# Performance work log

Measured on AMD Instinct MI355X. Metric: run time of the kernel, lower is better.

The kernel has to match this reference:

```python
import jax, jax.numpy as jnp
import numpy as np

N, E, C, H, G = 100000, 1600000, 128, 64, 512
TOL = 1e-7          # PyG topk tolerance
MIN_SCORE = 0.05
EPS_KL = 1e-14


def setup_inputs() -> dict:
    key = jax.random.key(0)
    ks = jax.random.split(key, 12)
    d = {}
    d["x"] = jax.random.normal(ks[0], (N, C), jnp.float32)
    d["edge_index"] = jax.random.randint(ks[1], (2, E), 0, N)
    d["batch"] = jnp.sort(jax.random.randint(ks[2], (N,), 0, G))
    d["attn"] = jax.random.uniform(ks[3], (N,), jnp.float32, minval=1e-3, maxval=1.0)
    def lin(k, i, o):
        return (jax.random.normal(k, (i, o), jnp.float32) / np.sqrt(i)).astype(jnp.float32)
    d["W1"] = lin(ks[4], C, H); d["b1"] = jnp.zeros((H,), jnp.float32)
    d["W2"] = lin(ks[5], H, H); d["b2"] = jnp.zeros((H,), jnp.float32)
    d["pool_w"] = (jax.random.normal(ks[6], (C,), jnp.float32) / np.sqrt(C)).astype(jnp.float32)
    d["W3"] = lin(ks[7], H, H); d["b3"] = jnp.zeros((H,), jnp.float32)
    d["W4"] = lin(ks[8], H, H); d["b4"] = jnp.zeros((H,), jnp.float32)
    d["Wl"] = lin(ks[9], H, 1); d["bl"] = jnp.zeros((1,), jnp.float32)
    return d


def _gin(x, src, dst, Wa, ba, Wb, bb, edge_w=None):
    # GINConv with eps=0: nn((1+0)*x + sum_{j in N(i)} x_j), nn = Lin-ReLU-Lin
    msg = x[src]                                   # [E, F] gather
    if edge_w is not None:
        msg = msg * edge_w[:, None]                # drop pruned edges
    agg = jax.ops.segment_sum(msg, dst, num_segments=x.shape[0])
    h = x + agg
    return jax.nn.relu(h @ Wa + ba) @ Wb + bb


def reference(x, edge_index, batch, attn, W1, b1, W2, b2, pool_w, W3, b3, W4, b4, Wl, bl):
    src, dst = edge_index[0], edge_index[1]
    out = jax.nn.relu(_gin(x, src, dst, W1, b1, W2, b2))

    # --- TopKPooling(min_score=0.05), attn=x ---
    raw = x @ pool_w                               # [N] attention logits
    m = jax.ops.segment_max(raw, batch, num_segments=G)
    e = jnp.exp(raw - m[batch])
    z = jax.ops.segment_sum(e, batch, num_segments=G)
    score = e / z[batch]                           # per-graph softmax
    smax = jax.ops.segment_max(score, batch, num_segments=G)
    thresh = jnp.minimum(smax[batch] - TOL, MIN_SCORE)
    mask = score > thresh                          # kept nodes (>=1 per graph)
    maskf = mask.astype(x.dtype)
    out = out * (score * maskf)[:, None]           # x[perm] * score[perm]
    edge_keep = maskf[src] * maskf[dst]            # filter_adj: both endpoints kept

    out = jax.nn.relu(_gin(out, src, dst, W3, b3, W4, b4, edge_w=edge_keep)) * maskf[:, None]
    graph_out = jax.ops.segment_sum(out, batch, num_segments=G)  # global_add_pool
    pred = (graph_out @ Wl + bl).reshape(-1)       # [G]

    # attn_loss = scatter_mean(kl_div(log(score+eps), attn[perm]), batch)
    kl = attn * (jnp.log(attn) - jnp.log(score + EPS_KL))
    cnt = jax.ops.segment_sum(maskf, batch, num_segments=G)
    attn_loss = jax.ops.segment_sum(kl * maskf, batch, num_segments=G) / jnp.maximum(cnt, 1.0)

    ratio = maskf.sum() / x.shape[0]
    return pred, attn_loss, ratio
```

## Files before the change

kernel.cpp:

```cpp
#include <hip/hip_runtime.h>
#include <math.h>

#define N_NODES 100000
#define N_EDGES 1600000
#define C_IN    128
#define H_DIM   64
#define G_GRAPHS 512
#define MAXG    4096
#define ELCAP   65536
#define KPG     32
#define NBITS   3136

__device__ __forceinline__ int lbound(const int* __restrict__ b, int val) {
    int lo = 0, hi = N_NODES;
    while (lo < hi) {
        int mid = (lo + hi) >> 1;
        if (b[mid] < val) lo = mid + 1; else hi = mid;
    }
    return lo;
}

__global__ void kpre(const float* __restrict__ x, const float* __restrict__ pool_w,
                     float* __restrict__ sc, unsigned int* __restrict__ zero_region) {
    int gid = blockIdx.x * blockDim.x + threadIdx.x;
    if (gid < NBITS + 1) zero_region[gid] = 0u;
    const int lane = threadIdx.x & 63;
    const int l32  = lane & 31;
    const int half = lane >> 5;
    const float4 pwv = ((const float4*)pool_w)[l32];
    const int wid = blockIdx.x * (blockDim.x >> 6) + (threadIdx.x >> 6);
    const int nw  = gridDim.x * (blockDim.x >> 6);
    for (int r0 = wid * 4; r0 < N_NODES; r0 += nw * 4) {
        int rowA = r0 + half;
        int rowB = r0 + 2 + half;
        float4 xa = ((const float4*)(x + (size_t)rowA * C_IN))[l32];
        float4 xb = ((const float4*)(x + (size_t)rowB * C_IN))[l32];
        float pa = xa.x * pwv.x + xa.y * pwv.y + xa.z * pwv.z + xa.w * pwv.w;
        float pb = xb.x * pwv.x + xb.y * pwv.y + xb.z * pwv.z + xb.w * pwv.w;
        #pragma unroll
        for (int m = 16; m > 0; m >>= 1) {
            pa += __shfl_xor(pa, m, 64);
            pb += __shfl_xor(pb, m, 64);
        }
        if (l32 == 0) { sc[rowA] = pa; sc[rowB] = pb; }
    }
}

__device__ __forceinline__ float blk_max(float v, float* red, int lane, int w) {
    #pragma unroll
    for (int m = 32; m > 0; m >>= 1) v = fmaxf(v, __shfl_xor(v, m, 64));
    if (lane == 0) red[w] = v;
    __syncthreads();
    float r = fmaxf(fmaxf(red[0], red[1]), fmaxf(red[2], red[3]));
    __syncthreads();
    return r;
}
__device__ __forceinline__ float blk_sum(float v, float* red, int lane, int w) {
    #pragma unroll
    for (int m = 32; m > 0; m >>= 1) v += __shfl_xor(v, m, 64);
    if (lane == 0) red[w] = v;
    __syncthreads();
    float r = (red[0] + red[1]) + (red[2] + red[3]);
    __syncthreads();
    return r;
}

__global__ void kA4(const int* __restrict__ batch, const float* __restrict__ attn,
                    float* __restrict__ sc, unsigned int* __restrict__ kept_bits,
                    int* __restrict__ klist, int* __restrict__ kcnt,
                    float* __restrict__ B, float* __restrict__ out) {
    __shared__ float buf[MAXG];
    __shared__ float red[4];
    __shared__ int   lst[KPG];
    __shared__ int   cntk;
    const int g = blockIdx.x;
    const int t = threadIdx.x;
    const int lane = t & 63;
    const int w = t >> 6;
    const int ns = lbound(batch, g);
    const int ne = lbound(batch, g + 1);
    const int cn = ne - ns;
    if (cn <= 0) {
        if (t == 0) { out[G_GRAPHS + g] = 0.f; kcnt[g] = 0; }
        return;
    }
    if (t == 0) cntk = 0;
    float lmax = -3.4e38f;
    for (int i = t; i < cn; i += 256) { float r = sc[ns + i]; buf[i] = r; lmax = fmaxf(lmax, r); }
    float m = blk_max(lmax, red, lane, w);
    float lsum = 0.f;
    for (int i = t; i < cn; i += 256) { float e = expf(buf[i] - m); buf[i] = e; lsum += e; }
    float z = blk_sum(lsum, red, lane, w);
    float thresh = fminf(1.f / z - 1e-7f, 0.05f);
    float klacc = 0.f;
    for (int i = t; i < cn; i += 256) {
        float s = buf[i] / z;
        if (s > thresh) {
            int n = ns + i;
            int p = atomicAdd(&cntk, 1);
            if (p < KPG) lst[p] = i;
            sc[n] = s;
            float a = attn[n];
            klacc += a * (logf(a) - logf(s + 1e-14f));
        }
    }
    float klsum = blk_sum(klacc, red, lane, w);
    int kct = cntk;
    int kc = kct < KPG ? kct : KPG;
    if (t == 0) {
        out[G_GRAPHS + g] = (kct > 0) ? klsum / (float)kct : 0.f;
        kcnt[g] = kc;
    }
    for (int i = t; i < kc; i += 256) {
        int n = ns + lst[i];
        klist[g * KPG + i] = n;
        atomicOr(&kept_bits[n >> 5], 1u << (n & 31));
    }
    for (int j = t; j < kc * H_DIM; j += 256)
        B[(size_t)(ns + lst[j >> 6]) * H_DIM + (j & 63)] = 0.f;
}

__device__ __forceinline__ void emit(bool hit, int s, int d, int* __restrict__ list,
                                     int cap, int* __restrict__ count, int lane) {
    unsigned long long bal = __ballot(hit);
    if (bal == 0ull) return;
    int leader = __ffsll((long long)bal) - 1;
    int cnt = __popcll(bal);
    int base = 0;
    if (lane == leader) base = atomicAdd(count, cnt);
    base = __shfl(base, leader, 64);
    if (hit) {
        int p = base + __popcll(bal & ((1ull << lane) - 1ull));
        if (p < cap) { list[p] = s; list[cap + p] = d; }
    }
}

__global__ void k5f2(const int* __restrict__ ei, const unsigned int* __restrict__ bits,
                     const float* __restrict__ x, const float* __restrict__ W1,
                     float* __restrict__ B, int* __restrict__ elsd,
                     int* __restrict__ elcount) {
    __shared__ float W1s[C_IN * H_DIM];
    __shared__ int ls[1024], ld[1024];
    __shared__ int c1;
    const int t = threadIdx.x;
    const int lane = t & 63;
    if (t == 0) c1 = 0;
    int t4 = blockIdx.x * 256 + t;
    bool valid = t4 < (N_EDGES / 4);
    int4 s4 = make_int4(0, 0, 0, 0), d4 = make_int4(0, 0, 0, 0);
    if (valid) {
        s4 = ((const int4*)ei)[t4];
        d4 = ((const int4*)(ei + N_EDGES))[t4];
    }
    __syncthreads();
    int sv[4] = {s4.x, s4.y, s4.z, s4.w};
    int dv[4] = {d4.x, d4.y, d4.z, d4.w};
    bool bk[4];
    #pragma unroll
    for (int q = 0; q < 4; ++q) {
        int ss = sv[q], dd = dv[q];
        bool kd = valid && (((bits[dd >> 5] >> (dd & 31)) & 1u) != 0u);
        bk[q] = kd && (((bits[ss >> 5] >> (ss & 31)) & 1u) != 0u);
        if (kd) { int p = atomicAdd(&c1, 1); ls[p] = ss; ld[p] = dd; }
    }
    #pragma unroll
    for (int q = 0; q < 4; ++q) emit(bk[q], sv[q], dv[q], elsd, ELCAP, elcount, lane);
    __syncthreads();
    const int nloc = c1;
    if (nloc == 0) return;
    for (int i = t; i < C_IN * H_DIM; i += 256) W1s[i] = W1[i];
    __syncthreads();
    const int w = t >> 6;
    for (int idx = w; idx < nloc; idx += 4) {
        int s = ls[idx];
        int d = ld[idx];
        const float4* xr = (const float4*)(x + (size_t)s * C_IN);
        float acc = 0.f;
        #pragma unroll 8
        for (int k4 = 0; k4 < C_IN / 4; ++k4) {
            float4 xv = xr[k4];
            acc = fmaf(xv.x, W1s[(4 * k4 + 0) * H_DIM + lane], acc);
            acc = fmaf(xv.y, W1s[(4 * k4 + 1) * H_DIM + lane], acc);
            acc = fmaf(xv.z, W1s[(4 * k4 + 2) * H_DIM + lane], acc);
            acc = fmaf(xv.w, W1s[(4 * k4 + 3) * H_DIM + lane], acc);
        }
        atomicAdd(&B[(size_t)d * H_DIM + lane], acc);
    }
}

__device__ __forceinline__ float computeA(int n, int lane,
                                          const float* __restrict__ x,
                                          const float* __restrict__ B,
                                          const float* __restrict__ sc,
                                          const float* __restrict__ W1, float b1l,
                                          const float* __restrict__ W2, float b2l,
                                          const float* __restrict__ W3) {
    const float4* xr = (const float4*)(x + (size_t)n * C_IN);
    float u = 0.f;
    #pragma unroll 8
    for (int k4 = 0; k4 < C_IN / 4; ++k4) {
        float4 xv = xr[k4];
        u = fmaf(xv.x, W1[(4 * k4 + 0) * H_DIM + lane], u);
        u = fmaf(xv.y, W1[(4 * k4 + 1) * H_DIM + lane], u);
        u = fmaf(xv.z, W1[(4 * k4 + 2) * H_DIM + lane], u);
        u = fmaf(xv.w, W1[(4 * k4 + 3) * H_DIM + lane], u);
    }
    float t1 = fmaxf(u + B[(size_t)n * H_DIM + lane] + b1l, 0.f);
    float o1 = b2l;
    #pragma unroll 8
    for (int k = 0; k < H_DIM; ++k) o1 = fmaf(__shfl(t1, k, 64), W2[k * H_DIM + lane], o1);
    o1 = fmaxf(o1, 0.f);
    float v = 0.f;
    #pragma unroll 8
    for (int k = 0; k < H_DIM; ++k) v = fmaf(__shfl(o1, k, 64), W3[k * H_DIM + lane], v);
    return v * sc[n];
}

__global__ void k8c(const int* __restrict__ klist, const int* __restrict__ kcnt,
                    const float* __restrict__ sc, const float* __restrict__ x,
                    const float* __restrict__ W1, const float* __restrict__ b1,
                    const float* __restrict__ W2, const float* __restrict__ b2,
                    const float* __restrict__ W3, const float* __restrict__ b3,
                    const float* __restrict__ W4, const float* __restrict__ b4,
                    const float* __restrict__ Wl, const float* __restrict__ bl,
                    const float* __restrict__ B, const int* __restrict__ elsd,
                    const int* __restrict__ elcount, float* __restrict__ out) {
    const int g = blockIdx.x;
    const int lane = threadIdx.x;
    const float b1l = b1[lane], b2l = b2[lane], b3l = b3[lane], b4l = b4[lane];
    const int kc = kcnt[g];
    int ec = *elcount; if (ec > ELCAP) ec = ELCAP;
    float gsum = 0.f;
    for (int i = 0; i < kc; ++i) {
        int n = __builtin_amdgcn_readfirstlane(klist[g * KPG + i]);
        float agg = 0.f;
        for (int base = 0; base < ec; base += 64) {
            int idx = base + lane;
            int dd = (idx < ec) ? elsd[ELCAP + idx] : -1;
            bool mtc = (dd == n);
            int ssl = mtc ? elsd[idx] : 0;
            unsigned long long bal = __ballot(mtc);
            while (bal) {
                int j = __ffsll((long long)bal) - 1;
                bal &= bal - 1;
                int s = __builtin_amdgcn_readfirstlane(__shfl(ssl, j, 64));
                agg += computeA(s, lane, x, B, sc, W1, b1l, W2, b2l, W3);
            }
        }
        float vA = computeA(n, lane, x, B, sc, W1, b1l, W2, b2l, W3);
        float t = fmaxf(vA + agg + b3l, 0.f);
        float o2 = b4l;
        #pragma unroll 8
        for (int k = 0; k < H_DIM; ++k) o2 = fmaf(__shfl(t, k, 64), W4[k * H_DIM + lane], o2);
        gsum += fmaxf(o2, 0.f);
    }
    float p = gsum * Wl[lane];
    #pragma unroll
    for (int m = 32; m > 0; m >>= 1) p += __shfl_xor(p, m, 64);
    if (lane == 0) out[g] = p + bl[0];
    if (g == 0) {
        int tot = 0;
        for (int i = lane; i < G_GRAPHS; i += 64) tot += kcnt[i];
        #pragma unroll
        for (int m = 32; m > 0; m >>= 1) tot += __shfl_xor(tot, m, 64);
        if (lane == 0) out[2 * G_GRAPHS] = (float)tot * (1.f / (float)N_NODES);
    }
}

extern "C" void kernel_launch(void* const* d_in, const int* in_sizes, int n_in,
                              void* d_out, int out_size, void* d_ws, size_t ws_size,
                              hipStream_t stream) {
    const float* x      = (const float*)d_in[0];
    const int*   ei     = (const int*)d_in[1];
    const int*   batch  = (const int*)d_in[2];
    const float* attn   = (const float*)d_in[3];
    const float* W1     = (const float*)d_in[4];
    const float* b1     = (const float*)d_in[5];
    const float* W2     = (const float*)d_in[6];
    const float* b2     = (const float*)d_in[7];
    const float* pool_w = (const float*)d_in[8];
    const float* W3     = (const float*)d_in[9];
    const float* b3     = (const float*)d_in[10];
    const float* W4     = (const float*)d_in[11];
    const float* b4     = (const float*)d_in[12];
    const float* Wl     = (const float*)d_in[13];
    const float* bl     = (const float*)d_in[14];
    float* out = (float*)d_out;

    float* B      = (float*)d_ws;
    float* sc     = B + (size_t)N_NODES * H_DIM;
    int*   klist  = (int*)(sc + N_NODES);
    int*   kcnt   = klist + G_GRAPHS * KPG;
    int*   elsd   = kcnt + G_GRAPHS;
    unsigned int* kept_bits = (unsigned int*)(elsd + 2 * ELCAP);
    int*          elcount   = (int*)(kept_bits + NBITS);

    kpre <<<2048, 256, 0, stream>>>(x, pool_w, sc, kept_bits);
    kA4  <<<G_GRAPHS, 256, 0, stream>>>(batch, attn, sc, kept_bits, klist, kcnt, B, out);
    k5f2 <<<(N_EDGES / 4 + 255) / 256, 256, 0, stream>>>(ei, kept_bits, x, W1, B,
                                                         elsd, elcount);
    k8c  <<<G_GRAPHS, 64, 0, stream>>>(klist, kcnt, sc, x, W1, b1, W2, b2, W3, b3,
                                       W4, b4, Wl, bl, B, elsd, elcount, out);
}
```

Baseline: 174.9 us.

## Fuse pooling, edge filtering and second GIN into one cooperative kernel

```diff
diff --git a/kernel.cpp b/kernel.cpp
--- a/kernel.cpp
+++ b/kernel.cpp
@@ -1,5 +1,8 @@
 #include <hip/hip_runtime.h>
+#include <hip/hip_cooperative_groups.h>
 #include <math.h>
+
+namespace cg = cooperative_groups;
 
 #define N_NODES 100000
 #define N_EDGES 1600000
@@ -9,21 +12,25 @@
 #define MAXG    4096
 #define ELCAP   65536
 #define KPG     32
-#define NBITS   3136
-
-__device__ __forceinline__ int lbound(const int* __restrict__ b, int val) {
-    int lo = 0, hi = N_NODES;
-    while (lo < hi) {
-        int mid = (lo + hi) >> 1;
-        if (b[mid] < val) lo = mid + 1; else hi = mid;
-    }
-    return lo;
-}
+#define MAGIC   0x5A17C0DE
 
 __global__ void kpre(const float* __restrict__ x, const float* __restrict__ pool_w,
-                     float* __restrict__ sc, unsigned int* __restrict__ zero_region) {
+                     const int* __restrict__ batch, float* __restrict__ sc,
+                     int* __restrict__ gstart) {
     int gid = blockIdx.x * blockDim.x + threadIdx.x;
-    if (gid < NBITS + 1) zero_region[gid] = 0u;
+    int nth = gridDim.x * blockDim.x;
+    for (int i = gid; i < N_NODES; i += nth) {
+        int bc = batch[i];
+        if (i == 0) {
+            for (int g = 0; g <= bc; ++g) gstart[g] = 0;
+        } else {
+            int bp = batch[i - 1];
+            for (int g = bp + 1; g <= bc; ++g) gstart[g] = i;
+        }
+        if (i == N_NODES - 1) {
+            for (int g = bc + 1; g <= G_GRAPHS; ++g) gstart[g] = N_NODES;
+        }
+    }
     const int lane = threadIdx.x & 63;
     const int l32  = lane & 31;
     const int half = lane >> 5;
@@ -46,7 +53,7 @@
     }
 }
 
-__device__ __forceinline__ float blk_max(float v, float* red, int lane, int w) {
+__device__ __forceinline__ float blk_max(float v, volatile float* red, int lane, int w) {
     #pragma unroll
     for (int m = 32; m > 0; m >>= 1) v = fmaxf(v, __shfl_xor(v, m, 64));
     if (lane == 0) red[w] = v;
@@ -55,7 +62,7 @@
     __syncthreads();
     return r;
 }
-__device__ __forceinline__ float blk_sum(float v, float* red, int lane, int w) {
+__device__ __forceinline__ float blk_sum(float v, volatile float* red, int lane, int w) {
     #pragma unroll
     for (int m = 32; m > 0; m >>= 1) v += __shfl_xor(v, m, 64);
     if (lane == 0) red[w] = v;
@@ -63,61 +70,6 @@
     float r = (red[0] + red[1]) + (red[2] + red[3]);
     __syncthreads();
     return r;
-}
-
-__global__ void kA4(const int* __restrict__ batch, const float* __restrict__ attn,
-                    float* __restrict__ sc, unsigned int* __restrict__ kept_bits,
-                    int* __restrict__ klist, int* __restrict__ kcnt,
-                    float* __restrict__ B, float* __restrict__ out) {
-    __shared__ float buf[MAXG];
-    __shared__ float red[4];
-    __shared__ int   lst[KPG];
-    __shared__ int   cntk;
-    const int g = blockIdx.x;
-    const int t = threadIdx.x;
-    const int lane = t & 63;
-    const int w = t >> 6;
-    const int ns = lbound(batch, g);
-    const int ne = lbound(batch, g + 1);
-    const int cn = ne - ns;
-    if (cn <= 0) {
-        if (t == 0) { out[G_GRAPHS + g] = 0.f; kcnt[g] = 0; }
-        return;
-    }
-    if (t == 0) cntk = 0;
-    float lmax = -3.4e38f;
-    for (int i = t; i < cn; i += 256) { float r = sc[ns + i]; buf[i] = r; lmax = fmaxf(lmax, r); }
-    float m = blk_max(lmax, red, lane, w);
-    float lsum = 0.f;
-    for (int i = t; i < cn; i += 256) { float e = expf(buf[i] - m); buf[i] = e; lsum += e; }
-    float z = blk_sum(lsum, red, lane, w);
-    float thresh = fminf(1.f / z - 1e-7f, 0.05f);
-    float klacc = 0.f;
-    for (int i = t; i < cn; i += 256) {
-        float s = buf[i] / z;
-        if (s > thresh) {
-            int n = ns + i;
-            int p = atomicAdd(&cntk, 1);
-            if (p < KPG) lst[p] = i;
-            sc[n] = s;
-            float a = attn[n];
-            klacc += a * (logf(a) - logf(s + 1e-14f));
-        }
-    }
-    float klsum = blk_sum(klacc, red, lane, w);
-    int kct = cntk;
-    int kc = kct < KPG ? kct : KPG;
-    if (t == 0) {
-        out[G_GRAPHS + g] = (kct > 0) ? klsum / (float)kct : 0.f;
-        kcnt[g] = kc;
-    }
-    for (int i = t; i < kc; i += 256) {
-        int n = ns + lst[i];
-        klist[g * KPG + i] = n;
-        atomicOr(&kept_bits[n >> 5], 1u << (n & 31));
-    }
-    for (int j = t; j < kc * H_DIM; j += 256)
-        B[(size_t)(ns + lst[j >> 6]) * H_DIM + (j & 63)] = 0.f;
 }
 
 __device__ __forceinline__ void emit(bool hit, int s, int d, int* __restrict__ list,
@@ -132,59 +84,6 @@
     if (hit) {
         int p = base + __popcll(bal & ((1ull << lane) - 1ull));
         if (p < cap) { list[p] = s; list[cap + p] = d; }
-    }
-}
-
-__global__ void k5f2(const int* __restrict__ ei, const unsigned int* __restrict__ bits,
-                     const float* __restrict__ x, const float* __restrict__ W1,
-                     float* __restrict__ B, int* __restrict__ elsd,
-                     int* __restrict__ elcount) {
-    __shared__ float W1s[C_IN * H_DIM];
-    __shared__ int ls[1024], ld[1024];
-    __shared__ int c1;
-    const int t = threadIdx.x;
-    const int lane = t & 63;
-    if (t == 0) c1 = 0;
-    int t4 = blockIdx.x * 256 + t;
-    bool valid = t4 < (N_EDGES / 4);
-    int4 s4 = make_int4(0, 0, 0, 0), d4 = make_int4(0, 0, 0, 0);
-    if (valid) {
-        s4 = ((const int4*)ei)[t4];
-        d4 = ((const int4*)(ei + N_EDGES))[t4];
-    }
-    __syncthreads();
-    int sv[4] = {s4.x, s4.y, s4.z, s4.w};
-    int dv[4] = {d4.x, d4.y, d4.z, d4.w};
-    bool bk[4];
-    #pragma unroll
-    for (int q = 0; q < 4; ++q) {
-        int ss = sv[q], dd = dv[q];
-        bool kd = valid && (((bits[dd >> 5] >> (dd & 31)) & 1u) != 0u);
-        bk[q] = kd && (((bits[ss >> 5] >> (ss & 31)) & 1u) != 0u);
-        if (kd) { int p = atomicAdd(&c1, 1); ls[p] = ss; ld[p] = dd; }
-    }
-    #pragma unroll
-    for (int q = 0; q < 4; ++q) emit(bk[q], sv[q], dv[q], elsd, ELCAP, elcount, lane);
-    __syncthreads();
-    const int nloc = c1;
-    if (nloc == 0) return;
-    for (int i = t; i < C_IN * H_DIM; i += 256) W1s[i] = W1[i];
-    __syncthreads();
-    const int w = t >> 6;
-    for (int idx = w; idx < nloc; idx += 4) {
-        int s = ls[idx];
-        int d = ld[idx];
-        const float4* xr = (const float4*)(x + (size_t)s * C_IN);
-        float acc = 0.f;
-        #pragma unroll 8
-        for (int k4 = 0; k4 < C_IN / 4; ++k4) {
-            float4 xv = xr[k4];
-            acc = fmaf(xv.x, W1s[(4 * k4 + 0) * H_DIM + lane], acc);
-            acc = fmaf(xv.y, W1s[(4 * k4 + 1) * H_DIM + lane], acc);
-            acc = fmaf(xv.z, W1s[(4 * k4 + 2) * H_DIM + lane], acc);
-            acc = fmaf(xv.w, W1s[(4 * k4 + 3) * H_DIM + lane], acc);
-        }
-        atomicAdd(&B[(size_t)d * H_DIM + lane], acc);
     }
 }
 
@@ -216,54 +115,166 @@
     return v * sc[n];
 }
 
-__global__ void k8c(const int* __restrict__ klist, const int* __restrict__ kcnt,
-                    const float* __restrict__ sc, const float* __restrict__ x,
-                    const float* __restrict__ W1, const float* __restrict__ b1,
-                    const float* __restrict__ W2, const float* __restrict__ b2,
-                    const float* __restrict__ W3, const float* __restrict__ b3,
-                    const float* __restrict__ W4, const float* __restrict__ b4,
-                    const float* __restrict__ Wl, const float* __restrict__ bl,
-                    const float* __restrict__ B, const int* __restrict__ elsd,
-                    const int* __restrict__ elcount, float* __restrict__ out) {
+__global__ __launch_bounds__(256, 2)
+void kcoop(const int* __restrict__ batch, const float* __restrict__ attn,
+           const float* __restrict__ x, const int* __restrict__ ei,
+           const float* __restrict__ W1, const float* __restrict__ b1,
+           const float* __restrict__ W2, const float* __restrict__ b2,
+           const float* __restrict__ W3, const float* __restrict__ b3,
+           const float* __restrict__ W4, const float* __restrict__ b4,
+           const float* __restrict__ Wl, const float* __restrict__ bl,
+           const int* __restrict__ gstart, float* __restrict__ sc,
+           int* __restrict__ flags, int* __restrict__ klist, int* __restrict__ kcnt,
+           int* __restrict__ elsd, int* __restrict__ elcount,
+           float* __restrict__ B, float* __restrict__ out) {
+    __shared__ float buf[MAXG];
+    __shared__ float red[4];
+    __shared__ int   lst[KPG];
+    __shared__ int   cntk;
+    cg::grid_group grid = cg::this_grid();
     const int g = blockIdx.x;
-    const int lane = threadIdx.x;
-    const float b1l = b1[lane], b2l = b2[lane], b3l = b3[lane], b4l = b4[lane];
-    const int kc = kcnt[g];
-    int ec = *elcount; if (ec > ELCAP) ec = ELCAP;
-    float gsum = 0.f;
-    for (int i = 0; i < kc; ++i) {
-        int n = __builtin_amdgcn_readfirstlane(klist[g * KPG + i]);
-        float agg = 0.f;
-        for (int base = 0; base < ec; base += 64) {
-            int idx = base + lane;
-            int dd = (idx < ec) ? elsd[ELCAP + idx] : -1;
-            bool mtc = (dd == n);
-            int ssl = mtc ? elsd[idx] : 0;
-            unsigned long long bal = __ballot(mtc);
-            while (bal) {
-                int j = __ffsll((long long)bal) - 1;
-                bal &= bal - 1;
-                int s = __builtin_amdgcn_readfirstlane(__shfl(ssl, j, 64));
-                agg += computeA(s, lane, x, B, sc, W1, b1l, W2, b2l, W3);
-            }
-        }
-        float vA = computeA(n, lane, x, B, sc, W1, b1l, W2, b2l, W3);
-        float t = fmaxf(vA + agg + b3l, 0.f);
-        float o2 = b4l;
-        #pragma unroll 8
-        for (int k = 0; k < H_DIM; ++k) o2 = fmaf(__shfl(t, k, 64), W4[k * H_DIM + lane], o2);
-        gsum += fmaxf(o2, 0.f);
-    }
-    float p = gsum * Wl[lane];
-    #pragma unroll
-    for (int m = 32; m > 0; m >>= 1) p += __shfl_xor(p, m, 64);
-    if (lane == 0) out[g] = p + bl[0];
-    if (g == 0) {
-        int tot = 0;
-        for (int i = lane; i < G_GRAPHS; i += 64) tot += kcnt[i];
-        #pragma unroll
-        for (int m = 32; m > 0; m >>= 1) tot += __shfl_xor(tot, m, 64);
-        if (lane == 0) out[2 * G_GRAPHS] = (float)tot * (1.f / (float)N_NODES);
+    const int t = threadIdx.x;
+    const int lane = t & 63;
+    const int w = t >> 6;
+
+    if (g == 0 && t == 0) *elcount = 0;
+    const int ns = gstart[g], ne = gstart[g + 1];
+    const int cn = ne - ns;
+    if (cn > 0) {
+        if (t == 0) cntk = 0;
+        float lmax = -3.4e38f;
+        for (int i = t; i < cn; i += 256) { float r = sc[ns + i]; buf[i] = r; lmax = fmaxf(lmax, r); }
+        float m = blk_max(lmax, red, lane, w);
+        float lsum = 0.f;
+        for (int i = t; i < cn; i += 256) { float e = expf(buf[i] - m); buf[i] = e; lsum += e; }
+        float z = blk_sum(lsum, red, lane, w);
+        float thresh = fminf(1.f / z - 1e-7f, 0.05f);
+        float klacc = 0.f;
+        for (int i = t; i < cn; i += 256) {
+            float s = buf[i] / z;
+            if (s > thresh) {
+                int n = ns + i;
+                int p = atomicAdd(&cntk, 1);
+                if (p < KPG) lst[p] = i;
+                sc[n] = s;
+                float a = attn[n];
+                klacc += a * (logf(a) - logf(s + 1e-14f));
+            }
+        }
+        float klsum = blk_sum(klacc, red, lane, w);
+        int kct = cntk;
+        int kc = kct < KPG ? kct : KPG;
+        if (t == 0) {
+            out[G_GRAPHS + g] = (kct > 0) ? klsum / (float)kct : 0.f;
+            kcnt[g] = kc;
+        }
+        for (int i = t; i < kc; i += 256) {
+            int n = ns + lst[i];
+            klist[g * KPG + i] = n;
+            flags[n] = MAGIC;
+        }
+        for (int j = t; j < kc * H_DIM; j += 256)
+            B[(size_t)(ns + lst[j >> 6]) * H_DIM + (j & 63)] = 0.f;
+    } else if (t == 0) {
+        out[G_GRAPHS + g] = 0.f;
+        kcnt[g] = 0;
+    }
+    grid.sync();
+
+    {
+        __shared__ int c1;
+        int* ls = (int*)buf;
+        int* ld = ls + 1024;
+        const int niter = (N_EDGES / 4 + 255) / 256;
+        for (int it = g; it < niter; it += G_GRAPHS) {
+            if (t == 0) c1 = 0;
+            __syncthreads();
+            int t4 = it * 256 + t;
+            bool valid = t4 < (N_EDGES / 4);
+            int4 s4 = make_int4(0, 0, 0, 0), d4 = make_int4(0, 0, 0, 0);
+            if (valid) {
+                s4 = ((const int4*)ei)[t4];
+                d4 = ((const int4*)(ei + N_EDGES))[t4];
+            }
+            int sv[4] = {s4.x, s4.y, s4.z, s4.w};
+            int dv[4] = {d4.x, d4.y, d4.z, d4.w};
+            bool bk[4];
+            #pragma unroll
+            for (int q = 0; q < 4; ++q) {
+                int ss = sv[q], dd = dv[q];
+                bool kd = valid && (flags[dd] == MAGIC);
+                bk[q] = kd && (flags[ss] == MAGIC);
+                if (kd) { int p = atomicAdd(&c1, 1); ls[p] = ss; ld[p] = dd; }
+            }
+            #pragma unroll
+            for (int q = 0; q < 4; ++q) emit(bk[q], sv[q], dv[q], elsd, ELCAP, elcount, lane);
+            __syncthreads();
+            const int nloc = c1;
+            for (int idx = w; idx < nloc; idx += 4) {
+                int s = ls[idx];
+                int d = ld[idx];
+                const float4* xr = (const float4*)(x + (size_t)s * C_IN);
+                float acc = 0.f;
+                #pragma unroll 8
+                for (int k4 = 0; k4 < C_IN / 4; ++k4) {
+                    float4 xv = xr[k4];
+                    acc = fmaf(xv.x, W1[(4 * k4 + 0) * H_DIM + lane], acc);
+                    acc = fmaf(xv.y, W1[(4 * k4 + 1) * H_DIM + lane], acc);
+                    acc = fmaf(xv.z, W1[(4 * k4 + 2) * H_DIM + lane], acc);
+                    acc = fmaf(xv.w, W1[(4 * k4 + 3) * H_DIM + lane], acc);
+                }
+                atomicAdd(&B[(size_t)d * H_DIM + lane], acc);
+            }
+            __syncthreads();
+        }
+    }
+    grid.sync();
+
+    {
+        const float b1l = b1[lane], b2l = b2[lane], b3l = b3[lane], b4l = b4[lane];
+        const int kc = kcnt[g];
+        int ec = *elcount; if (ec > ELCAP) ec = ELCAP;
+        float gsum = 0.f;
+        for (int i = w; i < kc; i += 4) {
+            int n = __builtin_amdgcn_readfirstlane(klist[g * KPG + i]);
+            float agg = 0.f;
+            for (int base = 0; base < ec; base += 64) {
+                int idx = base + lane;
+                int dd = (idx < ec) ? elsd[ELCAP + idx] : -1;
+                bool mtc = (dd == n);
+                int ssl = mtc ? elsd[idx] : 0;
+                unsigned long long bal = __ballot(mtc);
+                while (bal) {
+                    int j = __ffsll((long long)bal) - 1;
+                    bal &= bal - 1;
+                    int s = __builtin_amdgcn_readfirstlane(__shfl(ssl, j, 64));
+                    agg += computeA(s, lane, x, B, sc, W1, b1l, W2, b2l, W3);
+                }
+            }
+            float vA = computeA(n, lane, x, B, sc, W1, b1l, W2, b2l, W3);
+            float tt = fmaxf(vA + agg + b3l, 0.f);
+            float o2 = b4l;
+            #pragma unroll 8
+            for (int k = 0; k < H_DIM; ++k) o2 = fmaf(__shfl(tt, k, 64), W4[k * H_DIM + lane], o2);
+            gsum += fmaxf(o2, 0.f);
+        }
+        float* cred = buf;
+        cred[w * 64 + lane] = gsum;
+        __syncthreads();
+        if (w == 0) {
+            float tot = (cred[lane] + cred[64 + lane]) + (cred[128 + lane] + cred[192 + lane]);
+            float p = tot * Wl[lane];
+            #pragma unroll
+            for (int m = 32; m > 0; m >>= 1) p += __shfl_xor(p, m, 64);
+            if (lane == 0) out[g] = p + bl[0];
+            if (g == 0) {
+                int totk = 0;
+                for (int i = lane; i < G_GRAPHS; i += 64) totk += kcnt[i];
+                #pragma unroll
+                for (int m = 32; m > 0; m >>= 1) totk += __shfl_xor(totk, m, 64);
+                if (lane == 0) out[2 * G_GRAPHS] = (float)totk * (1.f / (float)N_NODES);
+            }
+        }
     }
 }
 
@@ -289,16 +300,22 @@
 
     float* B      = (float*)d_ws;
     float* sc     = B + (size_t)N_NODES * H_DIM;
-    int*   klist  = (int*)(sc + N_NODES);
+    int*   gstart = (int*)(sc + N_NODES);
+    int*   klist  = gstart + (G_GRAPHS + 1);
     int*   kcnt   = klist + G_GRAPHS * KPG;
     int*   elsd   = kcnt + G_GRAPHS;
-    unsigned int* kept_bits = (unsigned int*)(elsd + 2 * ELCAP);
-    int*          elcount   = (int*)(kept_bits + NBITS);
-
-    kpre <<<2048, 256, 0, stream>>>(x, pool_w, sc, kept_bits);
-    kA4  <<<G_GRAPHS, 256, 0, stream>>>(batch, attn, sc, kept_bits, klist, kcnt, B, out);
-    k5f2 <<<(N_EDGES / 4 + 255) / 256, 256, 0, stream>>>(ei, kept_bits, x, W1, B,
-                                                         elsd, elcount);
-    k8c  <<<G_GRAPHS, 64, 0, stream>>>(klist, kcnt, sc, x, W1, b1, W2, b2, W3, b3,
-                                       W4, b4, Wl, bl, B, elsd, elcount, out);
-}
+    int*   flags  = elsd + 2 * ELCAP;
+    int*   elcount = flags + N_NODES;
+
+    kpre<<<2048, 256, 0, stream>>>(x, pool_w, batch, sc, gstart);
+
+    void* params[] = {
+        (void*)&batch, (void*)&attn, (void*)&x, (void*)&ei,
+        (void*)&W1, (void*)&b1, (void*)&W2, (void*)&b2,
+        (void*)&W3, (void*)&b3, (void*)&W4, (void*)&b4,
+        (void*)&Wl, (void*)&bl,
+        (void*)&gstart, (void*)&sc, (void*)&flags, (void*)&klist, (void*)&kcnt,
+        (void*)&elsd, (void*)&elcount, (void*)&B, (void*)&out
+    };
+    hipLaunchCooperativeKernel((void*)kcoop, dim3(G_GRAPHS), dim3(256), params, 0, stream);
+}
```

After: 318.5 us. 82.1% more time.
